# Optimization experiments

Measured on AMD Instinct MI355X. Metric: run time of the kernel, lower is better.

Reference implementation:

```python
import jax, jax.numpy as jnp
import numpy as np

N_NODES = 100000
N_EDGES = 1600000
IN_C, HID_C, OUT_C = 128, 128, 40


def setup_inputs() -> dict:
    key = jax.random.key(0)
    ks = jax.random.split(key, 10)
    def lin(k, fin, fout):
        return jax.random.normal(k, (fin, fout), jnp.float32) / np.sqrt(fin).astype(np.float32)
    return {
        "x": jax.random.normal(ks[0], (N_NODES, IN_C), jnp.float32),
        "edge_index": jax.random.randint(ks[1], (2, N_EDGES), 0, N_NODES, jnp.int64),
        "W1a": lin(ks[2], IN_C, HID_C), "b1a": jnp.zeros((HID_C,), jnp.float32),
        "W1b": lin(ks[3], HID_C, HID_C), "b1b": jnp.zeros((HID_C,), jnp.float32),
        "W2a": lin(ks[4], HID_C, HID_C), "b2a": jnp.zeros((HID_C,), jnp.float32),
        "W2b": lin(ks[5], HID_C, OUT_C), "b2b": jnp.zeros((OUT_C,), jnp.float32),
    }


def gin_conv(x, edge_index, Wa, ba, Wb, bb):
    # GINConv with eps=0: h_i = MLP(x_i + sum_{j in N(i)} x_j)
    src, dst = edge_index[0], edge_index[1]
    agg = jax.ops.segment_sum(x[src], dst, num_segments=N_NODES)  # [N, C]
    h = x + agg
    h = jnp.maximum(h @ Wa + ba, 0.0)  # Linear + ReLU
    return h @ Wb + bb                 # Linear


def reference(x, edge_index, W1a, b1a, W1b, b1b, W2a, b2a, W2b, b2b):
    h = gin_conv(x, edge_index, W1a, b1a, W1b, b1b)
    h = jnp.maximum(h, 0.0)
    # dropout(p=0.5) treated as identity (eval mode / deterministic reference)
    h = gin_conv(h, edge_index, W2a, b2a, W2b, b2b)
    return jax.nn.log_softmax(h, axis=1)
```

## Files before the change

kernel.cpp:

```cpp
#include <hip/hip_runtime.h>

#define N_NODES 100000
#define N_EDGES 1600000
#define CH 128
#define OUTC 40
#define CAP 48
#define NBKT 98
#define BKT_CAP 18432
#define P1_EDGES 4096
#define ROW4 16
#define QROW2 16
#define QSCALE (6.5f / 127.0f)
#define QINV   (127.0f / 6.5f)
#define ZROW N_NODES
#define CONV_GRID 6250
#define BIN_GRID ((N_EDGES + P1_EDGES - 1) / P1_EDGES)

typedef __attribute__((ext_vector_type(8))) short bf16x8s;
typedef __attribute__((ext_vector_type(4))) float f32x4;

__device__ __forceinline__ unsigned short f2b_rne(float f) {
    union { float f; unsigned int u; } c; c.f = f;
    unsigned int r = (c.u + 0x7FFF + ((c.u >> 16) & 1)) >> 16;
    return (unsigned short)r;
}
__device__ __forceinline__ float b2f(unsigned short b) {
    union { float f; unsigned int u; } c; c.u = ((unsigned int)b) << 16;
    return c.f;
}
__device__ __forceinline__ int q8(float f) {
    return __float2int_rn(fminf(fmaxf(f * QINV, -127.f), 127.f));
}

__global__ __launch_bounds__(256) void conv_bin(const float4* __restrict__ in,
                                                ushort4* __restrict__ outb,
                                                uint2* __restrict__ outq, int n8,
                                                unsigned int* __restrict__ xqd,
                                                unsigned int* __restrict__ h1qd,
                                                const int* __restrict__ esrc,
                                                const int* __restrict__ edst,
                                                int* __restrict__ gcursor,
                                                unsigned int* __restrict__ bins) {
    __shared__ uint2 stage[P1_EDGES];
    __shared__ int lcnt[NBKT];
    __shared__ int lofs[NBKT];
    __shared__ int lpos[NBKT];
    __shared__ int gbase[NBKT];
    const int tid = threadIdx.x;

    if (blockIdx.x >= BIN_GRID) {
        const int cb = blockIdx.x - BIN_GRID;
        if (cb == 0) {
            if (tid >= 128 && tid < 160) {
                int i = tid - 128;
                xqd[(size_t)ZROW * 32 + i] = 0x80808080u;
                h1qd[(size_t)ZROW * 32 + i] = 0x80808080u;
            }
        }
        int i = cb * 256 + tid;
        if (i >= n8) return;
        float4 a = in[i * 2], b = in[i * 2 + 1];
        ushort4 o0, o1;
        o0.x = f2b_rne(a.x); o0.y = f2b_rne(a.y); o0.z = f2b_rne(a.z); o0.w = f2b_rne(a.w);
        o1.x = f2b_rne(b.x); o1.y = f2b_rne(b.y); o1.z = f2b_rne(b.z); o1.w = f2b_rne(b.w);
        outb[i * 2] = o0; outb[i * 2 + 1] = o1;
        uint2 q;
        q.x = (unsigned)((q8(a.x) + 128) & 0xFF) | (((unsigned)((q8(a.y) + 128) & 0xFF)) << 8) |
              (((unsigned)((q8(a.z) + 128) & 0xFF)) << 16) | (((unsigned)((q8(a.w) + 128) & 0xFF)) << 24);
        q.y = (unsigned)((q8(b.x) + 128) & 0xFF) | (((unsigned)((q8(b.y) + 128) & 0xFF)) << 8) |
              (((unsigned)((q8(b.z) + 128) & 0xFF)) << 16) | (((unsigned)((q8(b.w) + 128) & 0xFF)) << 24);
        outq[i] = q;
        return;
    }

    const int e0 = blockIdx.x * P1_EDGES;

    for (int i = tid; i < NBKT; i += 256) lcnt[i] = 0;
    __syncthreads();

    int s[16], d[16];
#pragma unroll
    for (int i = 0; i < 16; ++i) {
        int e = e0 + i * 256 + tid;
        if (e < N_EDGES) { s[i] = esrc[e]; d[i] = edst[e]; }
        else d[i] = -1;
    }
#pragma unroll
    for (int i = 0; i < 16; ++i)
        if (d[i] >= 0) atomicAdd(&lcnt[d[i] >> 10], 1);
    __syncthreads();

    if (tid < NBKT) lofs[tid] = lcnt[tid];
    __syncthreads();
    for (int dd = 1; dd < NBKT; dd <<= 1) {
        int v = 0;
        if (tid < NBKT && tid >= dd) v = lofs[tid - dd];
        __syncthreads();
        if (tid < NBKT) lofs[tid] += v;
        __syncthreads();
    }
    if (tid < NBKT) {
        lpos[tid] = lofs[tid] - lcnt[tid];
        gbase[tid] = atomicAdd(&gcursor[tid], lcnt[tid]);
    }
    __syncthreads();

#pragma unroll
    for (int i = 0; i < 16; ++i) {
        if (d[i] >= 0) {
            int b = d[i] >> 10;
            int slot = atomicAdd(&lpos[b], 1);
            stage[slot] = make_uint2((unsigned)s[i], (unsigned)d[i]);
        }
    }
    __syncthreads();

    int total = lofs[NBKT - 1];
    for (int r = tid; r < total; r += 256) {
        uint2 rec = stage[r];
        int b = (int)(rec.y >> 10);
        int excl = lofs[b] - lcnt[b];
        int pos = gbase[b] + (r - excl);
        unsigned p = ((rec.y & 1023u) << 17) | rec.x;
        if (pos < BKT_CAP) bins[(size_t)b * BKT_CAP + pos] = p;
    }
}

__global__ __launch_bounds__(1024) void build_pack(const unsigned int* __restrict__ bins,
                                                   const int* __restrict__ gcursor,
                                                   int* __restrict__ adj,
                                                   int* __restrict__ cnt,
                                                   const float* __restrict__ W0,
                                                   const float* __restrict__ W1,
                                                   const float* __restrict__ W2,
                                                   const float* __restrict__ Wo,
                                                   unsigned short* __restrict__ P0,
                                                   unsigned short* __restrict__ P1,
                                                   unsigned short* __restrict__ P2,
                                                   unsigned short* __restrict__ Po) {
    __shared__ int lc[1024];
    const int tid = threadIdx.x;
    if (blockIdx.x >= NBKT) {
        int t = (blockIdx.x - NBKT) * 1024 + tid;
        if (t < 3 * 2048) {
            int which = t >> 11;
            int rem = t & 2047;
            int lane = rem & 63;
            int ks = (rem >> 6) & 3;
            int nt = rem >> 8;
            const float* W = which == 0 ? W0 : (which == 1 ? W1 : W2);
            unsigned short* P = which == 0 ? P0 : (which == 1 ? P1 : P2);
            int n = nt * 16 + (lane & 15);
            int kbase = ks * 32 + (lane >> 4) * 8;
            unsigned short* dst = P + ((nt * 4 + ks) * 64 + lane) * 8;
#pragma unroll
            for (int j = 0; j < 8; ++j)
                dst[j] = f2b_rne(W[(kbase + j) * CH + n]);
        } else if (t < 3 * 2048 + 768) {
            int u = t - 3 * 2048;
            int nt = u >> 8, rem = u & 255;
            int ks = rem >> 6, lane = rem & 63;
            int n = nt * 16 + (lane & 15);
            int kbase = ks * 32 + (lane >> 4) * 8;
            unsigned short* dst = Po + ((nt * 4 + ks) * 64 + lane) * 8;
#pragma unroll
            for (int j = 0; j < 8; ++j)
                dst[j] = (n < OUTC) ? f2b_rne(Wo[(kbase + j) * OUTC + n]) : (unsigned short)0;
        }
        return;
    }
    const int b = blockIdx.x;
    const int base = b << 10;
    lc[tid] = 0;
    __syncthreads();
    int n = gcursor[b]; if (n > BKT_CAP) n = BKT_CAP;
    const unsigned int* myb = bins + (size_t)b * BKT_CAP;
    for (int i = tid; i < n; i += 1024) {
        unsigned p = myb[i];
        int local = (int)(p >> 17);
        int src = (int)(p & 0x1FFFFu);
        int slot = atomicAdd(&lc[local], 1);
        if (slot < CAP) adj[(base + local) * CAP + slot] = src;
    }
    __syncthreads();
    {
        int node = base + tid;
        if (node < N_NODES) cnt[node] = lc[tid];
    }
}

__device__ __forceinline__ void gather_epi(unsigned a0, unsigned a1, unsigned a2, unsigned a3,
                                           uint4 sv, int bias, float dq, uint4* __restrict__ dst) {
    float q0 = (float)((int)(a0 & 0xFFFFu) - bias);
    float q1 = (float)((int)(a1 & 0xFFFFu) - bias);
    float q2 = (float)((int)(a0 >> 16) - bias);
    float q3 = (float)((int)(a1 >> 16) - bias);
    float q4 = (float)((int)(a2 & 0xFFFFu) - bias);
    float q5 = (float)((int)(a3 & 0xFFFFu) - bias);
    float q6 = (float)((int)(a2 >> 16) - bias);
    float q7 = (float)((int)(a3 >> 16) - bias);
    float r0 = b2f((unsigned short)(sv.x & 0xFFFF)) + dq * q0;
    float r1 = b2f((unsigned short)(sv.x >> 16)) + dq * q1;
    float r2 = b2f((unsigned short)(sv.y & 0xFFFF)) + dq * q2;
    float r3 = b2f((unsigned short)(sv.y >> 16)) + dq * q3;
    float r4 = b2f((unsigned short)(sv.z & 0xFFFF)) + dq * q4;
    float r5 = b2f((unsigned short)(sv.z >> 16)) + dq * q5;
    float r6 = b2f((unsigned short)(sv.w & 0xFFFF)) + dq * q6;
    float r7 = b2f((unsigned short)(sv.w >> 16)) + dq * q7;
    uint4 o;
    o.x = (unsigned)f2b_rne(r0) | ((unsigned)f2b_rne(r1) << 16);
    o.y = (unsigned)f2b_rne(r2) | ((unsigned)f2b_rne(r3) << 16);
    o.z = (unsigned)f2b_rne(r4) | ((unsigned)f2b_rne(r5) << 16);
    o.w = (unsigned)f2b_rne(r6) | ((unsigned)f2b_rne(r7) << 16);
    *dst = o;
}

template <bool FIXED>
__device__ __forceinline__ void gather_u8_body(const unsigned int* __restrict__ xq,
                                               const unsigned short* __restrict__ xb,
                                               const int* __restrict__ adj,
                                               const int* __restrict__ cnt,
                                               const unsigned int* __restrict__ hmax,
                                               unsigned short* __restrict__ agg) {
    const int wave = threadIdx.x >> 6;
    const int lane = threadIdx.x & 63;
    const int node0 = blockIdx.x * 8 + wave * 2;
    const int grp = lane >> 4, l16 = lane & 15;
    const uint2* q2 = reinterpret_cast<const uint2*>(xq);
    const uint4* f4 = reinterpret_cast<const uint4*>(xb);

    int2 dgp = *reinterpret_cast<const int2*>(cnt + node0);
    int deg0 = dgp.x > CAP ? CAP : dgp.x;
    int deg1 = dgp.y > CAP ? CAP : dgp.y;
    int nr0 = (deg0 + 15) & ~15;
    int nr1 = (deg1 + 15) & ~15;
    int nrm = nr0 > nr1 ? nr0 : nr1;
    int nb0 = (lane < deg0) ? adj[node0 * CAP + lane] : ZROW;
    int nb1 = (lane < deg1) ? adj[(node0 + 1) * CAP + lane] : ZROW;

    float dq;
    if (FIXED) dq = QSCALE;
    else {
        union { unsigned u; float f; } c; c.u = hmax[0];
        dq = c.f * (1.0f / 127.0f);
    }

    unsigned a00 = 0, a01 = 0, a02 = 0, a03 = 0;
    unsigned a10 = 0, a11 = 0, a12 = 0, a13 = 0;

    for (int j = 0; j < nrm; j += 16) {
        int j0 = j + grp;
        int s00 = __shfl(nb0, j0, 64);
        int s01 = __shfl(nb0, j0 + 4, 64);
        int s02 = __shfl(nb0, j0 + 8, 64);
        int s03 = __shfl(nb0, j0 + 12, 64);
        int s10 = __shfl(nb1, j0, 64);
        int s11 = __shfl(nb1, j0 + 4, 64);
        int s12 = __shfl(nb1, j0 + 8, 64);
        int s13 = __shfl(nb1, j0 + 12, 64);
        uint2 v00 = q2[s00 * QROW2 + l16];
        uint2 v01 = q2[s01 * QROW2 + l16];
        uint2 v02 = q2[s02 * QROW2 + l16];
        uint2 v03 = q2[s03 * QROW2 + l16];
        uint2 v10 = q2[s10 * QROW2 + l16];
        uint2 v11 = q2[s11 * QROW2 + l16];
        uint2 v12 = q2[s12 * QROW2 + l16];
        uint2 v13 = q2[s13 * QROW2 + l16];
        a00 += __builtin_amdgcn_perm(v00.x, v00.x, 0x0C020C00u);
        a01 += __builtin_amdgcn_perm(v00.x, v00.x, 0x0C030C01u);
        a02 += __builtin_amdgcn_perm(v00.y, v00.y, 0x0C020C00u);
        a03 += __builtin_amdgcn_perm(v00.y, v00.y, 0x0C030C01u);
        a00 += __builtin_amdgcn_perm(v01.x, v01.x, 0x0C020C00u);
        a01 += __builtin_amdgcn_perm(v01.x, v01.x, 0x0C030C01u);
        a02 += __builtin_amdgcn_perm(v01.y, v01.y, 0x0C020C00u);
        a03 += __builtin_amdgcn_perm(v01.y, v01.y, 0x0C030C01u);
        a00 += __builtin_amdgcn_perm(v02.x, v02.x, 0x0C020C00u);
        a01 += __builtin_amdgcn_perm(v02.x, v02.x, 0x0C030C01u);
        a02 += __builtin_amdgcn_perm(v02.y, v02.y, 0x0C020C00u);
        a03 += __builtin_amdgcn_perm(v02.y, v02.y, 0x0C030C01u);
        a00 += __builtin_amdgcn_perm(v03.x, v03.x, 0x0C020C00u);
        a01 += __builtin_amdgcn_perm(v03.x, v03.x, 0x0C030C01u);
        a02 += __builtin_amdgcn_perm(v03.y, v03.y, 0x0C020C00u);
        a03 += __builtin_amdgcn_perm(v03.y, v03.y, 0x0C030C01u);
        a10 += __builtin_amdgcn_perm(v10.x, v10.x, 0x0C020C00u);
        a11 += __builtin_amdgcn_perm(v10.x, v10.x, 0x0C030C01u);
        a12 += __builtin_amdgcn_perm(v10.y, v10.y, 0x0C020C00u);
        a13 += __builtin_amdgcn_perm(v10.y, v10.y, 0x0C030C01u);
        a10 += __builtin_amdgcn_perm(v11.x, v11.x, 0x0C020C00u);
        a11 += __builtin_amdgcn_perm(v11.x, v11.x, 0x0C030C01u);
        a12 += __builtin_amdgcn_perm(v11.y, v11.y, 0x0C020C00u);
        a13 += __builtin_amdgcn_perm(v11.y, v11.y, 0x0C030C01u);
        a10 += __builtin_amdgcn_perm(v12.x, v12.x, 0x0C020C00u);
        a11 += __builtin_amdgcn_perm(v12.x, v12.x, 0x0C030C01u);
        a12 += __builtin_amdgcn_perm(v12.y, v12.y, 0x0C020C00u);
        a13 += __builtin_amdgcn_perm(v12.y, v12.y, 0x0C030C01u);
        a10 += __builtin_amdgcn_perm(v13.x, v13.x, 0x0C020C00u);
        a11 += __builtin_amdgcn_perm(v13.x, v13.x, 0x0C030C01u);
        a12 += __builtin_amdgcn_perm(v13.y, v13.y, 0x0C020C00u);
        a13 += __builtin_amdgcn_perm(v13.y, v13.y, 0x0C030C01u);
    }
    a00 += (unsigned)__shfl_xor((int)a00, 16, 64); a00 += (unsigned)__shfl_xor((int)a00, 32, 64);
    a01 += (unsigned)__shfl_xor((int)a01, 16, 64); a01 += (unsigned)__shfl_xor((int)a01, 32, 64);
    a02 += (unsigned)__shfl_xor((int)a02, 16, 64); a02 += (unsigned)__shfl_xor((int)a02, 32, 64);
    a03 += (unsigned)__shfl_xor((int)a03, 16, 64); a03 += (unsigned)__shfl_xor((int)a03, 32, 64);
    a10 += (unsigned)__shfl_xor((int)a10, 16, 64); a10 += (unsigned)__shfl_xor((int)a10, 32, 64);
    a11 += (unsigned)__shfl_xor((int)a11, 16, 64); a11 += (unsigned)__shfl_xor((int)a11, 32, 64);
    a12 += (unsigned)__shfl_xor((int)a12, 16, 64); a12 += (unsigned)__shfl_xor((int)a12, 32, 64);
    a13 += (unsigned)__shfl_xor((int)a13, 16, 64); a13 += (unsigned)__shfl_xor((int)a13, 32, 64);

    uint4 sv0 = f4[node0 * ROW4 + l16];
    uint4 sv1 = f4[node0 * ROW4 + ROW4 + l16];

    if (grp == 0) {
        int bias = nrm << 7;
        uint4* dst = reinterpret_cast<uint4*>(agg);
        gather_epi(a00, a01, a02, a03, sv0, bias, dq, dst + node0 * ROW4 + l16);
        gather_epi(a10, a11, a12, a13, sv1, bias, dq, dst + node0 * ROW4 + ROW4 + l16);
    }
}

__global__ __launch_bounds__(256) void gather_agg_u8(const unsigned int* __restrict__ xq,
                                                     const unsigned short* __restrict__ xb,
                                                     const int* __restrict__ adj,
                                                     const int* __restrict__ cnt,
                                                     unsigned short* __restrict__ agg) {
    gather_u8_body<true>(xq, xb, adj, cnt, nullptr, agg);
}

__global__ __launch_bounds__(256) void gather_agg_u8_dyn(const unsigned int* __restrict__ xq,
                                                         const unsigned short* __restrict__ xb,
                                                         const int* __restrict__ adj,
                                                         const int* __restrict__ cnt,
                                                         const unsigned int* __restrict__ hmax,
                                                         unsigned short* __restrict__ agg) {
    gather_u8_body<false>(xq, xb, adj, cnt, hmax, agg);
}

__global__ __launch_bounds__(256) void quant_h1(const uint4* __restrict__ h1,
                                                const unsigned int* __restrict__ hmax,
                                                uint2* __restrict__ outq, int n8) {
    int i = blockIdx.x * 256 + threadIdx.x;
    if (i >= n8) return;
    union { unsigned u; float f; } c; c.u = hmax[0];
    float inv = 127.0f / fmaxf(c.f, 1e-30f);
    uint4 v = h1[i];
    int q[8];
    q[0] = __float2int_rn(fminf(b2f((unsigned short)(v.x & 0xFFFF)) * inv, 127.f));
    q[1] = __float2int_rn(fminf(b2f((unsigned short)(v.x >> 16)) * inv, 127.f));
    q[2] = __float2int_rn(fminf(b2f((unsigned short)(v.y & 0xFFFF)) * inv, 127.f));
    q[3] = __float2int_rn(fminf(b2f((unsigned short)(v.y >> 16)) * inv, 127.f));
    q[4] = __float2int_rn(fminf(b2f((unsigned short)(v.z & 0xFFFF)) * inv, 127.f));
    q[5] = __float2int_rn(fminf(b2f((unsigned short)(v.z >> 16)) * inv, 127.f));
    q[6] = __float2int_rn(fminf(b2f((unsigned short)(v.w & 0xFFFF)) * inv, 127.f));
    q[7] = __float2int_rn(fminf(b2f((unsigned short)(v.w >> 16)) * inv, 127.f));
    uint2 o;
    o.x = (unsigned)((q[0] + 128) & 0xFF) | (((unsigned)((q[1] + 128) & 0xFF)) << 8) |
          (((unsigned)((q[2] + 128) & 0xFF)) << 16) | (((unsigned)((q[3] + 128) & 0xFF)) << 24);
    o.y = (unsigned)((q[4] + 128) & 0xFF) | (((unsigned)((q[5] + 128) & 0xFF)) << 8) |
          (((unsigned)((q[6] + 128) & 0xFF)) << 16) | (((unsigned)((q[7] + 128) & 0xFF)) << 24);
    outq[i] = o;
}

__global__ __launch_bounds__(256) void gin_mlp_fused(const unsigned short* __restrict__ A,
                                                     const unsigned short* __restrict__ Pa,
                                                     const float* __restrict__ ba,
                                                     const unsigned short* __restrict__ Pb2,
                                                     const float* __restrict__ bb,
                                                     unsigned short* __restrict__ Cout,
                                                     unsigned int* __restrict__ hmax,
                                                     int M) {
    __shared__ unsigned short As[64 * 136];
    __shared__ float sm_max[4];
    const int row0 = blockIdx.x * 64;
    const int tid = threadIdx.x;
    const int wave = tid >> 6;
    const int lane = tid & 63;
    const int quad = lane >> 4;
    const int l15 = lane & 15;
    const int nt0 = wave * 2;

    bf16x8s b1f[2][4];
#pragma unroll
    for (int c = 0; c < 2; ++c)
#pragma unroll
        for (int ks = 0; ks < 4; ++ks)
            b1f[c][ks] = *reinterpret_cast<const bf16x8s*>(
                Pa + (((nt0 + c) * 4 + ks) * 64 + lane) * 8);

    {
        int r = tid & 63, seg = tid >> 6;
        int row = row0 + r;
        uint4 z = make_uint4(0, 0, 0, 0);
        const uint4* src = reinterpret_cast<const uint4*>(A + (long long)row * CH + seg * 32);
        uint4* dst = reinterpret_cast<uint4*>(&As[r * 136 + seg * 32]);
#pragma unroll
        for (int i = 0; i < 4; ++i)
            dst[i] = (row < M) ? src[i] : z;
    }
    __syncthreads();

    f32x4 acc[2][4];
#pragma unroll
    for (int c = 0; c < 2; ++c)
#pragma unroll
        for (int t = 0; t < 4; ++t) acc[c][t] = (f32x4){0.f, 0.f, 0.f, 0.f};
#pragma unroll
    for (int t = 0; t < 4; ++t)
#pragma unroll
        for (int ks = 0; ks < 4; ++ks) {
            bf16x8s af = *reinterpret_cast<const bf16x8s*>(
                &As[(t * 16 + l15) * 136 + ks * 32 + quad * 8]);
            acc[0][t] = __builtin_amdgcn_mfma_f32_16x16x32_bf16(af, b1f[0][ks], acc[0][t], 0, 0, 0);
            acc[1][t] = __builtin_amdgcn_mfma_f32_16x16x32_bf16(af, b1f[1][ks], acc[1][t], 0, 0, 0);
        }

    bf16x8s b2f_[2][4];
#pragma unroll
    for (int c = 0; c < 2; ++c)
#pragma unroll
        for (int ks = 0; ks < 4; ++ks)
            b2f_[c][ks] = *reinterpret_cast<const bf16x8s*>(
                Pb2 + (((nt0 + c) * 4 + ks) * 64 + lane) * 8);

    __syncthreads();
#pragma unroll
    for (int c = 0; c < 2; ++c) {
        int col = (nt0 + c) * 16 + l15;
        float bv = ba[col];
#pragma unroll
        for (int t = 0; t < 4; ++t)
#pragma unroll
            for (int r = 0; r < 4; ++r) {
                int rl = t * 16 + quad * 4 + r;
                As[rl * 136 + col] = f2b_rne(fmaxf(acc[c][t][r] + bv, 0.f));
            }
    }
    __syncthreads();

    f32x4 a2[2][4];
#pragma unroll
    for (int c = 0; c < 2; ++c)
#pragma unroll
        for (int t = 0; t < 4; ++t) a2[c][t] = (f32x4){0.f, 0.f, 0.f, 0.f};
#pragma unroll
    for (int t = 0; t < 4; ++t)
#pragma unroll
        for (int ks = 0; ks < 4; ++ks) {
            bf16x8s af = *reinterpret_cast<const bf16x8s*>(
                &As[(t * 16 + l15) * 136 + ks * 32 + quad * 8]);
            a2[0][t] = __builtin_amdgcn_mfma_f32_16x16x32_bf16(af, b2f_[0][ks], a2[0][t], 0, 0, 0);
            a2[1][t] = __builtin_amdgcn_mfma_f32_16x16x32_bf16(af, b2f_[1][ks], a2[1][t], 0, 0, 0);
        }
    __syncthreads();

    float wmax = 0.f;
#pragma unroll
    for (int c = 0; c < 2; ++c) {
        int col = (nt0 + c) * 16 + l15;
        float bv = bb[col];
#pragma unroll
        for (int t = 0; t < 4; ++t)
#pragma unroll
            for (int r = 0; r < 4; ++r) {
                int rl = t * 16 + quad * 4 + r;
                float v = fmaxf(a2[c][t][r] + bv, 0.f);
                if (row0 + rl < M) wmax = fmaxf(wmax, v);
                As[rl * 136 + col] = f2b_rne(v);
            }
    }
#pragma unroll
    for (int off = 1; off < 64; off <<= 1) wmax = fmaxf(wmax, __shfl_xor(wmax, off, 64));
    if (lane == 0) sm_max[wave] = wmax;
    __syncthreads();

    {
        int r = tid >> 2;
        int q = tid & 3;
        int row = row0 + r;
        if (row < M) {
            uint4* dst = reinterpret_cast<uint4*>(Cout + (long long)row * CH + q * 32);
            const unsigned short* sp = &As[r * 136 + q * 32];
#pragma unroll
            for (int i = 0; i < 4; ++i)
                dst[i] = *reinterpret_cast<const uint4*>(sp + i * 8);
        }
        if (tid == 0)
            atomicMax(hmax, __float_as_uint(fmaxf(fmaxf(sm_max[0], sm_max[1]),
                                                  fmaxf(sm_max[2], sm_max[3]))));
    }
}

__global__ __launch_bounds__(256) void gin_out_fused(const unsigned short* __restrict__ A,
                                                     const unsigned short* __restrict__ Pa,
                                                     const float* __restrict__ ba,
                                                     const unsigned short* __restrict__ Pb,
                                                     const float* __restrict__ bias,
                                                     float* __restrict__ out, int M) {
    __shared__ unsigned short As[64 * 136];
    const int row0 = blockIdx.x * 64;
    const int tid = threadIdx.x;
    const int wave = tid >> 6;
    const int lane = tid & 63;
    const int quad = lane >> 4;
    const int l15 = lane & 15;
    const int nt0 = wave * 2;

    bf16x8s b1f[2][4];
#pragma unroll
    for (int c = 0; c < 2; ++c)
#pragma unroll
        for (int ks = 0; ks < 4; ++ks)
            b1f[c][ks] = *reinterpret_cast<const bf16x8s*>(
                Pa + (((nt0 + c) * 4 + ks) * 64 + lane) * 8);

    {
        int r = tid & 63, seg = tid >> 6;
        int row = row0 + r;
        uint4 z = make_uint4(0, 0, 0, 0);
        const uint4* src = reinterpret_cast<const uint4*>(A + (long long)row * CH + seg * 32);
        uint4* dst = reinterpret_cast<uint4*>(&As[r * 136 + seg * 32]);
#pragma unroll
        for (int i = 0; i < 4; ++i)
            dst[i] = (row < M) ? src[i] : z;
    }
    __syncthreads();

    f32x4 acc[2][4];
#pragma unroll
    for (int c = 0; c < 2; ++c)
#pragma unroll
        for (int t = 0; t < 4; ++t) acc[c][t] = (f32x4){0.f, 0.f, 0.f, 0.f};
#pragma unroll
    for (int t = 0; t < 4; ++t)
#pragma unroll
        for (int ks = 0; ks < 4; ++ks) {
            bf16x8s af = *reinterpret_cast<const bf16x8s*>(
                &As[(t * 16 + l15) * 136 + ks * 32 + quad * 8]);
            acc[0][t] = __builtin_amdgcn_mfma_f32_16x16x32_bf16(af, b1f[0][ks], acc[0][t], 0, 0, 0);
            acc[1][t] = __builtin_amdgcn_mfma_f32_16x16x32_bf16(af, b1f[1][ks], acc[1][t], 0, 0, 0);
        }

    bf16x8s bof[3][4];
#pragma unroll
    for (int nt = 0; nt < 3; ++nt)
#pragma unroll
        for (int ks = 0; ks < 4; ++ks)
            bof[nt][ks] = *reinterpret_cast<const bf16x8s*>(
                Pb + ((nt * 4 + ks) * 64 + lane) * 8);

    __syncthreads();
#pragma unroll
    for (int c = 0; c < 2; ++c) {
        int col = (nt0 + c) * 16 + l15;
        float bv = ba[col];
#pragma unroll
        for (int t = 0; t < 4; ++t)
#pragma unroll
            for (int r = 0; r < 4; ++r) {
                int rl = t * 16 + quad * 4 + r;
                As[rl * 136 + col] = f2b_rne(fmaxf(acc[c][t][r] + bv, 0.f));
            }
    }
    __syncthreads();

    f32x4 oacc[3];
#pragma unroll
    for (int nt = 0; nt < 3; ++nt) oacc[nt] = (f32x4){0.f, 0.f, 0.f, 0.f};
#pragma unroll
    for (int ks = 0; ks < 4; ++ks) {
        bf16x8s af = *reinterpret_cast<const bf16x8s*>(
            &As[(wave * 16 + l15) * 136 + ks * 32 + quad * 8]);
#pragma unroll
        for (int nt = 0; nt < 3; ++nt)
            oacc[nt] = __builtin_amdgcn_mfma_f32_16x16x32_bf16(af, bof[nt][ks], oacc[nt], 0, 0, 0);
    }

    const float b0v = bias[l15];
    const float b1v = bias[16 + l15];
    const float b2v = (l15 < 8) ? bias[32 + l15] : 0.f;
#pragma unroll
    for (int r = 0; r < 4; ++r) {
        int row = row0 + wave * 16 + quad * 4 + r;
        float v0 = oacc[0][r] + b0v;
        float v1 = oacc[1][r] + b1v;
        float v2 = (l15 < 8) ? (oacc[2][r] + b2v) : -1e30f;
        float m = fmaxf(fmaxf(v0, v1), v2);
#pragma unroll
        for (int off = 1; off < 16; off <<= 1) m = fmaxf(m, __shfl_xor(m, off, 64));
        float s = __expf(v0 - m) + __expf(v1 - m) + ((l15 < 8) ? __expf(v2 - m) : 0.f);
#pragma unroll
        for (int off = 1; off < 16; off <<= 1) s += __shfl_xor(s, off, 64);
        float lg = m + __logf(s);
        if (row < M) {
            float* orow = out + (long long)row * OUTC;
            orow[l15] = v0 - lg;
            orow[16 + l15] = v1 - lg;
            if (l15 < 8) orow[32 + l15] = v2 - lg;
        }
    }
}

extern "C" void kernel_launch(void* const* d_in, const int* in_sizes, int n_in,
                              void* d_out, int out_size, void* d_ws, size_t ws_size,
                              hipStream_t stream) {
    const float* x   = (const float*)d_in[0];
    const int* eidx  = (const int*)d_in[1];
    const int* esrc  = eidx;
    const int* edst  = eidx + N_EDGES;
    const float* W1a = (const float*)d_in[2];
    const float* b1a = (const float*)d_in[3];
    const float* W1b = (const float*)d_in[4];
    const float* b1b = (const float*)d_in[5];
    const float* W2a = (const float*)d_in[6];
    const float* b2a = (const float*)d_in[7];
    const float* W2b = (const float*)d_in[8];
    const float* b2b = (const float*)d_in[9];
    float* out = (float*)d_out;

    const size_t fe = (size_t)N_NODES * CH;
    const size_t qrow_pad = 32;
    unsigned short* xb  = (unsigned short*)d_ws;
    unsigned short* b0  = xb + fe;
    unsigned short* b1  = b0 + fe;
    unsigned int* xq    = (unsigned int*)(b1 + fe);
    unsigned int* h1q   = xq + fe / 4 + qrow_pad;
    int* adj     = (int*)(h1q + fe / 4 + qrow_pad);
    int* cnt     = adj + (size_t)N_NODES * CAP;
    int* gcursor = cnt + N_NODES;
    unsigned int* hmax = (unsigned int*)(gcursor + NBKT);
    unsigned int* bins = (unsigned int*)(hmax + 2);
    unsigned short* P1 = (unsigned short*)(bins + (size_t)NBKT * BKT_CAP);
    unsigned short* P2 = P1 + 16384;
    unsigned short* P3 = P2 + 16384;
    unsigned short* Pb = P3 + 16384;

    const int gath_grid = N_NODES / 8;
    const int gemm_grid = (N_NODES + 63) / 64;
    const int q8_grid   = (int)((fe / 8 + 255) / 256);

    hipMemsetAsync(gcursor, 0, (NBKT + 2) * sizeof(int), stream);

    conv_bin<<<BIN_GRID + CONV_GRID, 256, 0, stream>>>(
        (const float4*)x, (ushort4*)xb, (uint2*)xq, (int)(fe / 8),
        xq, h1q, esrc, edst, gcursor, bins);
    build_pack<<<NBKT + 7, 1024, 0, stream>>>(bins, gcursor, adj, cnt,
                                              W1a, W1b, W2a, W2b, P1, P2, P3, Pb);

    gather_agg_u8<<<gath_grid, 256, 0, stream>>>(xq, xb, adj, cnt, b0);
    gin_mlp_fused<<<gemm_grid, 256, 0, stream>>>(b0, P1, b1a, P2, b1b, b1, hmax, N_NODES);

    quant_h1<<<q8_grid, 256, 0, stream>>>((const uint4*)b1, hmax, (uint2*)h1q, (int)(fe / 8));
    gather_agg_u8_dyn<<<gath_grid, 256, 0, stream>>>(h1q, b1, adj, cnt, hmax, b0);
    gin_out_fused<<<gemm_grid, 256, 0, stream>>>(b0, P3, b2a, Pb, b2b, out, N_NODES);
}
```

Measured before the change: 272.4 us.

## Process two 64-row tiles per block with register prefetch of second tile

```diff
diff --git a/kernel.cpp b/kernel.cpp
--- a/kernel.cpp
+++ b/kernel.cpp
@@ -371,13 +371,15 @@
                                                      int M) {
     __shared__ unsigned short As[64 * 136];
     __shared__ float sm_max[4];
-    const int row0 = blockIdx.x * 64;
+    const int row0 = blockIdx.x * 128;
     const int tid = threadIdx.x;
     const int wave = tid >> 6;
     const int lane = tid & 63;
     const int quad = lane >> 4;
     const int l15 = lane & 15;
     const int nt0 = wave * 2;
+    const int sr = tid & 63, sseg = tid >> 6;
+    const uint4 z = make_uint4(0, 0, 0, 0);
 
     bf16x8s b1f[2][4];
 #pragma unroll
@@ -388,31 +390,13 @@
                 Pa + (((nt0 + c) * 4 + ks) * 64 + lane) * 8);
 
     {
-        int r = tid & 63, seg = tid >> 6;
-        int row = row0 + r;
-        uint4 z = make_uint4(0, 0, 0, 0);
-        const uint4* src = reinterpret_cast<const uint4*>(A + (long long)row * CH + seg * 32);
-        uint4* dst = reinterpret_cast<uint4*>(&As[r * 136 + seg * 32]);
+        int row = row0 + sr;
+        const uint4* src = reinterpret_cast<const uint4*>(A + (long long)row * CH + sseg * 32);
+        uint4* dst = reinterpret_cast<uint4*>(&As[sr * 136 + sseg * 32]);
 #pragma unroll
         for (int i = 0; i < 4; ++i)
             dst[i] = (row < M) ? src[i] : z;
     }
-    __syncthreads();
-
-    f32x4 acc[2][4];
-#pragma unroll
-    for (int c = 0; c < 2; ++c)
-#pragma unroll
-        for (int t = 0; t < 4; ++t) acc[c][t] = (f32x4){0.f, 0.f, 0.f, 0.f};
-#pragma unroll
-    for (int t = 0; t < 4; ++t)
-#pragma unroll
-        for (int ks = 0; ks < 4; ++ks) {
-            bf16x8s af = *reinterpret_cast<const bf16x8s*>(
-                &As[(t * 16 + l15) * 136 + ks * 32 + quad * 8]);
-            acc[0][t] = __builtin_amdgcn_mfma_f32_16x16x32_bf16(af, b1f[0][ks], acc[0][t], 0, 0, 0);
-            acc[1][t] = __builtin_amdgcn_mfma_f32_16x16x32_bf16(af, b1f[1][ks], acc[1][t], 0, 0, 0);
-        }
 
     bf16x8s b2f_[2][4];
 #pragma unroll
@@ -421,73 +405,108 @@
         for (int ks = 0; ks < 4; ++ks)
             b2f_[c][ks] = *reinterpret_cast<const bf16x8s*>(
                 Pb2 + (((nt0 + c) * 4 + ks) * 64 + lane) * 8);
-
-    __syncthreads();
-#pragma unroll
-    for (int c = 0; c < 2; ++c) {
-        int col = (nt0 + c) * 16 + l15;
-        float bv = ba[col];
-#pragma unroll
-        for (int t = 0; t < 4; ++t)
-#pragma unroll
-            for (int r = 0; r < 4; ++r) {
-                int rl = t * 16 + quad * 4 + r;
-                As[rl * 136 + col] = f2b_rne(fmaxf(acc[c][t][r] + bv, 0.f));
+    __syncthreads();
+
+    float wmax = 0.f;
+    uint4 r1[4];
+#pragma unroll
+    for (int t = 0; t < 2; ++t) {
+        if (t == 1) {
+            __syncthreads();
+            uint4* dst = reinterpret_cast<uint4*>(&As[sr * 136 + sseg * 32]);
+#pragma unroll
+            for (int i = 0; i < 4; ++i) dst[i] = r1[i];
+            __syncthreads();
+        } else {
+            int row = row0 + 64 + sr;
+            const uint4* src = reinterpret_cast<const uint4*>(A + (long long)row * CH + sseg * 32);
+#pragma unroll
+            for (int i = 0; i < 4; ++i) r1[i] = (row < M) ? src[i] : z;
+        }
+
+        f32x4 acc[2][4];
+#pragma unroll
+        for (int c = 0; c < 2; ++c)
+#pragma unroll
+            for (int u = 0; u < 4; ++u) acc[c][u] = (f32x4){0.f, 0.f, 0.f, 0.f};
+#pragma unroll
+        for (int u = 0; u < 4; ++u)
+#pragma unroll
+            for (int ks = 0; ks < 4; ++ks) {
+                bf16x8s af = *reinterpret_cast<const bf16x8s*>(
+                    &As[(u * 16 + l15) * 136 + ks * 32 + quad * 8]);
+                acc[0][u] = __builtin_amdgcn_mfma_f32_16x16x32_bf16(af, b1f[0][ks], acc[0][u], 0, 0, 0);
+                acc[1][u] = __builtin_amdgcn_mfma_f32_16x16x32_bf16(af, b1f[1][ks], acc[1][u], 0, 0, 0);
             }
-    }
-    __syncthreads();
-
-    f32x4 a2[2][4];
-#pragma unroll
-    for (int c = 0; c < 2; ++c)
-#pragma unroll
-        for (int t = 0; t < 4; ++t) a2[c][t] = (f32x4){0.f, 0.f, 0.f, 0.f};
-#pragma unroll
-    for (int t = 0; t < 4; ++t)
-#pragma unroll
-        for (int ks = 0; ks < 4; ++ks) {
-            bf16x8s af = *reinterpret_cast<const bf16x8s*>(
-                &As[(t * 16 + l15) * 136 + ks * 32 + quad * 8]);
-            a2[0][t] = __builtin_amdgcn_mfma_f32_16x16x32_bf16(af, b2f_[0][ks], a2[0][t], 0, 0, 0);
-            a2[1][t] = __builtin_amdgcn_mfma_f32_16x16x32_bf16(af, b2f_[1][ks], a2[1][t], 0, 0, 0);
-        }
-    __syncthreads();
-
-    float wmax = 0.f;
-#pragma unroll
-    for (int c = 0; c < 2; ++c) {
-        int col = (nt0 + c) * 16 + l15;
-        float bv = bb[col];
-#pragma unroll
-        for (int t = 0; t < 4; ++t)
-#pragma unroll
-            for (int r = 0; r < 4; ++r) {
-                int rl = t * 16 + quad * 4 + r;
-                float v = fmaxf(a2[c][t][r] + bv, 0.f);
-                if (row0 + rl < M) wmax = fmaxf(wmax, v);
-                As[rl * 136 + col] = f2b_rne(v);
+        __syncthreads();
+
+#pragma unroll
+        for (int c = 0; c < 2; ++c) {
+            int col = (nt0 + c) * 16 + l15;
+            float bv = ba[col];
+#pragma unroll
+            for (int u = 0; u < 4; ++u)
+#pragma unroll
+                for (int r = 0; r < 4; ++r) {
+                    int rl = u * 16 + quad * 4 + r;
+                    As[rl * 136 + col] = f2b_rne(fmaxf(acc[c][u][r] + bv, 0.f));
+                }
+        }
+        __syncthreads();
+
+        f32x4 a2[2][4];
+#pragma unroll
+        for (int c = 0; c < 2; ++c)
+#pragma unroll
+            for (int u = 0; u < 4; ++u) a2[c][u] = (f32x4){0.f, 0.f, 0.f, 0.f};
+#pragma unroll
+        for (int u = 0; u < 4; ++u)
+#pragma unroll
+            for (int ks = 0; ks < 4; ++ks) {
+                bf16x8s af = *reinterpret_cast<const bf16x8s*>(
+                    &As[(u * 16 + l15) * 136 + ks * 32 + quad * 8]);
+                a2[0][u] = __builtin_amdgcn_mfma_f32_16x16x32_bf16(af, b2f_[0][ks], a2[0][u], 0, 0, 0);
+                a2[1][u] = __builtin_amdgcn_mfma_f32_16x16x32_bf16(af, b2f_[1][ks], a2[1][u], 0, 0, 0);
             }
-    }
+        __syncthreads();
+
+#pragma unroll
+        for (int c = 0; c < 2; ++c) {
+            int col = (nt0 + c) * 16 + l15;
+            float bv = bb[col];
+#pragma unroll
+            for (int u = 0; u < 4; ++u)
+#pragma unroll
+                for (int r = 0; r < 4; ++r) {
+                    int rl = u * 16 + quad * 4 + r;
+                    float v = fmaxf(a2[c][u][r] + bv, 0.f);
+                    if (row0 + t * 64 + rl < M) wmax = fmaxf(wmax, v);
+                    As[rl * 136 + col] = f2b_rne(v);
+                }
+        }
+        __syncthreads();
+
+        {
+            int cr = tid >> 2;
+            int cq = tid & 3;
+            int row = row0 + t * 64 + cr;
+            if (row < M) {
+                uint4* dst = reinterpret_cast<uint4*>(Cout + (long long)row * CH + cq * 32);
+                const unsigned short* sp = &As[cr * 136 + cq * 32];
+#pragma unroll
+                for (int i = 0; i < 4; ++i)
+                    dst[i] = *reinterpret_cast<const uint4*>(sp + i * 8);
+            }
+        }
+    }
+
 #pragma unroll
     for (int off = 1; off < 64; off <<= 1) wmax = fmaxf(wmax, __shfl_xor(wmax, off, 64));
     if (lane == 0) sm_max[wave] = wmax;
     __syncthreads();
-
-    {
-        int r = tid >> 2;
-        int q = tid & 3;
-        int row = row0 + r;
-        if (row < M) {
-            uint4* dst = reinterpret_cast<uint4*>(Cout + (long long)row * CH + q * 32);
-            const unsigned short* sp = &As[r * 136 + q * 32];
-#pragma unroll
-            for (int i = 0; i < 4; ++i)
-                dst[i] = *reinterpret_cast<const uint4*>(sp + i * 8);
-        }
-        if (tid == 0)
-            atomicMax(hmax, __float_as_uint(fmaxf(fmaxf(sm_max[0], sm_max[1]),
-                                                  fmaxf(sm_max[2], sm_max[3]))));
-    }
+    if (tid == 0)
+        atomicMax(hmax, __float_as_uint(fmaxf(fmaxf(sm_max[0], sm_max[1]),
+                                              fmaxf(sm_max[2], sm_max[3]))));
 }
 
 __global__ __launch_bounds__(256) void gin_out_fused(const unsigned short* __restrict__ A,
@@ -497,13 +516,15 @@
                                                      const float* __restrict__ bias,
                                                      float* __restrict__ out, int M) {
     __shared__ unsigned short As[64 * 136];
-    const int row0 = blockIdx.x * 64;
+    const int row0 = blockIdx.x * 128;
     const int tid = threadIdx.x;
     const int wave = tid >> 6;
     const int lane = tid & 63;
     const int quad = lane >> 4;
     const int l15 = lane & 15;
     const int nt0 = wave * 2;
+    const int sr = tid & 63, sseg = tid >> 6;
+    const uint4 z = make_uint4(0, 0, 0, 0);
 
     bf16x8s b1f[2][4];
 #pragma unroll
@@ -514,31 +535,13 @@
                 Pa + (((nt0 + c) * 4 + ks) * 64 + lane) * 8);
 
     {
-        int r = tid & 63, seg = tid >> 6;
-        int row = row0 + r;
-        uint4 z = make_uint4(0, 0, 0, 0);
-        const uint4* src = reinterpret_cast<const uint4*>(A + (long long)row * CH + seg * 32);
-        uint4* dst = reinterpret_cast<uint4*>(&As[r * 136 + seg * 32]);
+        int row = row0 + sr;
+        const uint4* src = reinterpret_cast<const uint4*>(A + (long long)row * CH + sseg * 32);
+        uint4* dst = reinterpret_cast<uint4*>(&As[sr * 136 + sseg * 32]);
 #pragma unroll
         for (int i = 0; i < 4; ++i)
             dst[i] = (row < M) ? src[i] : z;
     }
-    __syncthreads();
-
-    f32x4 acc[2][4];
-#pragma unroll
-    for (int c = 0; c < 2; ++c)
-#pragma unroll
-        for (int t = 0; t < 4; ++t) acc[c][t] = (f32x4){0.f, 0.f, 0.f, 0.f};
-#pragma unroll
-    for (int t = 0; t < 4; ++t)
-#pragma unroll
-        for (int ks = 0; ks < 4; ++ks) {
-            bf16x8s af = *reinterpret_cast<const bf16x8s*>(
-                &As[(t * 16 + l15) * 136 + ks * 32 + quad * 8]);
-            acc[0][t] = __builtin_amdgcn_mfma_f32_16x16x32_bf16(af, b1f[0][ks], acc[0][t], 0, 0, 0);
-            acc[1][t] = __builtin_amdgcn_mfma_f32_16x16x32_bf16(af, b1f[1][ks], acc[1][t], 0, 0, 0);
-        }
 
     bf16x8s bof[3][4];
 #pragma unroll
@@ -547,55 +550,89 @@
         for (int ks = 0; ks < 4; ++ks)
             bof[nt][ks] = *reinterpret_cast<const bf16x8s*>(
                 Pb + ((nt * 4 + ks) * 64 + lane) * 8);
-
-    __syncthreads();
-#pragma unroll
-    for (int c = 0; c < 2; ++c) {
-        int col = (nt0 + c) * 16 + l15;
-        float bv = ba[col];
-#pragma unroll
-        for (int t = 0; t < 4; ++t)
-#pragma unroll
-            for (int r = 0; r < 4; ++r) {
-                int rl = t * 16 + quad * 4 + r;
-                As[rl * 136 + col] = f2b_rne(fmaxf(acc[c][t][r] + bv, 0.f));
-            }
-    }
-    __syncthreads();
-
-    f32x4 oacc[3];
-#pragma unroll
-    for (int nt = 0; nt < 3; ++nt) oacc[nt] = (f32x4){0.f, 0.f, 0.f, 0.f};
-#pragma unroll
-    for (int ks = 0; ks < 4; ++ks) {
-        bf16x8s af = *reinterpret_cast<const bf16x8s*>(
-            &As[(wave * 16 + l15) * 136 + ks * 32 + quad * 8]);
-#pragma unroll
-        for (int nt = 0; nt < 3; ++nt)
-            oacc[nt] = __builtin_amdgcn_mfma_f32_16x16x32_bf16(af, bof[nt][ks], oacc[nt], 0, 0, 0);
-    }
+    __syncthreads();
 
     const float b0v = bias[l15];
     const float b1v = bias[16 + l15];
     const float b2v = (l15 < 8) ? bias[32 + l15] : 0.f;
-#pragma unroll
-    for (int r = 0; r < 4; ++r) {
-        int row = row0 + wave * 16 + quad * 4 + r;
-        float v0 = oacc[0][r] + b0v;
-        float v1 = oacc[1][r] + b1v;
-        float v2 = (l15 < 8) ? (oacc[2][r] + b2v) : -1e30f;
-        float m = fmaxf(fmaxf(v0, v1), v2);
-#pragma unroll
-        for (int off = 1; off < 16; off <<= 1) m = fmaxf(m, __shfl_xor(m, off, 64));
-        float s = __expf(v0 - m) + __expf(v1 - m) + ((l15 < 8) ? __expf(v2 - m) : 0.f);
-#pragma unroll
-        for (int off = 1; off < 16; off <<= 1) s += __shfl_xor(s, off, 64);
-        float lg = m + __logf(s);
-        if (row < M) {
-            float* orow = out + (long long)row * OUTC;
-            orow[l15] = v0 - lg;
-            orow[16 + l15] = v1 - lg;
-            if (l15 < 8) orow[32 + l15] = v2 - lg;
+
+    uint4 r1[4];
+#pragma unroll
+    for (int t = 0; t < 2; ++t) {
+        if (t == 1) {
+            __syncthreads();
+            uint4* dst = reinterpret_cast<uint4*>(&As[sr * 136 + sseg * 32]);
+#pragma unroll
+            for (int i = 0; i < 4; ++i) dst[i] = r1[i];
+            __syncthreads();
+        } else {
+            int row = row0 + 64 + sr;
+            const uint4* src = reinterpret_cast<const uint4*>(A + (long long)row * CH + sseg * 32);
+#pragma unroll
+            for (int i = 0; i < 4; ++i) r1[i] = (row < M) ? src[i] : z;
+        }
+
+        f32x4 acc[2][4];
+#pragma unroll
+        for (int c = 0; c < 2; ++c)
+#pragma unroll
+            for (int u = 0; u < 4; ++u) acc[c][u] = (f32x4){0.f, 0.f, 0.f, 0.f};
+#pragma unroll
+        for (int u = 0; u < 4; ++u)
+#pragma unroll
+            for (int ks = 0; ks < 4; ++ks) {
+                bf16x8s af = *reinterpret_cast<const bf16x8s*>(
+                    &As[(u * 16 + l15) * 136 + ks * 32 + quad * 8]);
+                acc[0][u] = __builtin_amdgcn_mfma_f32_16x16x32_bf16(af, b1f[0][ks], acc[0][u], 0, 0, 0);
+                acc[1][u] = __builtin_amdgcn_mfma_f32_16x16x32_bf16(af, b1f[1][ks], acc[1][u], 0, 0, 0);
+            }
+        __syncthreads();
+
+#pragma unroll
+        for (int c = 0; c < 2; ++c) {
+            int col = (nt0 + c) * 16 + l15;
+            float bv = ba[col];
+#pragma unroll
+            for (int u = 0; u < 4; ++u)
+#pragma unroll
+                for (int r = 0; r < 4; ++r) {
+                    int rl = u * 16 + quad * 4 + r;
+                    As[rl * 136 + col] = f2b_rne(fmaxf(acc[c][u][r] + bv, 0.f));
+                }
+        }
+        __syncthreads();
+
+        f32x4 oacc[3];
+#pragma unroll
+        for (int nt = 0; nt < 3; ++nt) oacc[nt] = (f32x4){0.f, 0.f, 0.f, 0.f};
+#pragma unroll
+        for (int ks = 0; ks < 4; ++ks) {
+            bf16x8s af = *reinterpret_cast<const bf16x8s*>(
+                &As[(wave * 16 + l15) * 136 + ks * 32 + quad * 8]);
+#pragma unroll
+            for (int nt = 0; nt < 3; ++nt)
+                oacc[nt] = __builtin_amdgcn_mfma_f32_16x16x32_bf16(af, bof[nt][ks], oacc[nt], 0, 0, 0);
+        }
+
+#pragma unroll
+        for (int r = 0; r < 4; ++r) {
+            int row = row0 + t * 64 + wave * 16 + quad * 4 + r;
+            float v0 = oacc[0][r] + b0v;
+            float v1 = oacc[1][r] + b1v;
+            float v2 = (l15 < 8) ? (oacc[2][r] + b2v) : -1e30f;
+            float m = fmaxf(fmaxf(v0, v1), v2);
+#pragma unroll
+            for (int off = 1; off < 16; off <<= 1) m = fmaxf(m, __shfl_xor(m, off, 64));
+            float s = __expf(v0 - m) + __expf(v1 - m) + ((l15 < 8) ? __expf(v2 - m) : 0.f);
+#pragma unroll
+            for (int off = 1; off < 16; off <<= 1) s += __shfl_xor(s, off, 64);
+            float lg = m + __logf(s);
+            if (row < M) {
+                float* orow = out + (long long)row * OUTC;
+                orow[l15] = v0 - lg;
+                orow[16 + l15] = v1 - lg;
+                if (l15 < 8) orow[32 + l15] = v2 - lg;
+            }
         }
     }
 }
@@ -635,7 +672,7 @@
     unsigned short* Pb = P3 + 16384;
 
     const int gath_grid = N_NODES / 8;
-    const int gemm_grid = (N_NODES + 63) / 64;
+    const int gemm_grid = (N_NODES + 127) / 128;
     const int q8_grid   = (int)((fe / 8 + 255) / 256);
 
     hipMemsetAsync(gcursor, 0, (NBKT + 2) * sizeof(int), stream);
```

After: 280.3 us. 2.9% more time.
